# Kernel tuning notes

Measured on AMD Instinct MI355X. Metric: run time of the kernel, lower is better.

The kernel has to match this reference:

```python
import jax, jax.numpy as jnp
import numpy as np

B, T, E, H, D = 4, 2048, 1024, 16, 64  # batch, seq(block_size), n_embed, num_heads, hidden_dim


def setup_inputs() -> dict:
    key = jax.random.key(0)
    ks = jax.random.split(key, 10)
    s_in = 1.0 / np.sqrt(E)
    return {
        "x": jax.random.normal(ks[0], (B, T, E), dtype=jnp.float32),
        "Wq": jax.random.normal(ks[1], (H, E, D), dtype=jnp.float32) * s_in,
        "bq": jnp.zeros((H, D), dtype=jnp.float32),
        "Wk": jax.random.normal(ks[2], (H, E, D), dtype=jnp.float32) * s_in,
        "bk": jnp.zeros((H, D), dtype=jnp.float32),
        "Wv": jax.random.normal(ks[3], (H, E, D), dtype=jnp.float32) * s_in,
        "bv": jnp.zeros((H, D), dtype=jnp.float32),
        "Wp": jax.random.normal(ks[4], (E, E), dtype=jnp.float32) * s_in,
        "bp": jnp.zeros((E,), dtype=jnp.float32),
    }


def reference(x, Wq, bq, Wk, bk, Wv, bv, Wp, bp):
    # Batched equivalent of the per-head Python loop: each head h computes
    # causal scaled-dot-product attention with its own Q/K/V projections.
    q = jnp.einsum("bte,hed->bhtd", x, Wq) + bq[None, :, None, :]
    k = jnp.einsum("bte,hed->bhtd", x, Wk) + bk[None, :, None, :]
    v = jnp.einsum("bte,hed->bhtd", x, Wv) + bv[None, :, None, :]
    scale = 1.0 / jnp.sqrt(jnp.asarray(D, dtype=x.dtype))
    scores = jnp.einsum("bhtd,bhsd->bhts", q, k) * scale  # [B,H,T,T]
    causal = jnp.tril(jnp.ones((T, T), dtype=bool))
    scores = jnp.where(causal[None, None, :, :], scores, jnp.asarray(-jnp.inf, dtype=x.dtype))
    att = jax.nn.softmax(scores, axis=-1)
    head_out = jnp.einsum("bhts,bhsd->bhtd", att, v)  # [B,H,T,D]
    # concat heads along last dim: [B,T,H*D] == [B,T,E]
    cat = head_out.transpose(0, 2, 1, 3).reshape(B, T, H * D)
    out = cat @ Wp + bp  # final projection (dropout is identity in eval)
    return out
```

## Files before the change

kernel.cpp:

```cpp
#include <hip/hip_runtime.h>


typedef __attribute__((ext_vector_type(8))) __bf16 bf16x8;
typedef __attribute__((ext_vector_type(4))) float f32x4;
typedef __attribute__((ext_vector_type(16))) float f32x16;
typedef __attribute__((ext_vector_type(4))) unsigned int u32x4;
typedef __attribute__((ext_vector_type(2))) unsigned int u32x2;
typedef unsigned short u16;
typedef unsigned int u32;

#define DEV __device__ __forceinline__

#define QK_SCALE 0.18033688011112042f

DEV u16 f2bf(float f) {
  u32 u = __builtin_bit_cast(u32, f);
  u += 0x7fffu + ((u >> 16) & 1u);
  return (u16)(u >> 16);
}
DEV u32 pack2(float a, float b) { return (u32)f2bf(a) | ((u32)f2bf(b) << 16); }

DEV float exp2_hw(float x) { float r; asm("v_exp_f32 %0, %1" : "=v"(r) : "v"(x)); return r; }
DEV u32 cvtpk_bf16(float lo, float hi) {
  u32 r; asm("v_cvt_pk_bf16_f32 %0, %1, %2" : "=v"(r) : "v"(lo), "v"(hi)); return r;
}
DEV void pl32swap(u32& a, u32& b) { asm("v_permlane32_swap_b32 %0, %1" : "+v"(a), "+v"(b)); }
DEV float max3f(float a, float b, float c) {
  float r; asm("v_max3_f32 %0, %1, %2, %3" : "=v"(r) : "v"(a), "v"(b), "v"(c)); return r;
}

DEV f32x16 zero16() { f32x16 z;
#pragma unroll
  for (int i = 0; i < 16; i++) z[i] = 0.f;
  return z; }

__global__ __launch_bounds__(256) void prep_x_kernel(
    const float* __restrict__ x, const float* __restrict__ bq, const float* __restrict__ bk,
    const float* __restrict__ bv, u16* __restrict__ xbf, float* __restrict__ bqkv) {
  int gid = blockIdx.x * 256 + threadIdx.x;
  if (gid < 3072) {
    float v = (gid < 1024) ? bq[gid] * QK_SCALE : (gid < 2048 ? bk[gid - 1024] : bv[gid - 2048]);
    bqkv[gid] = v;
  }
  const float4* xv = (const float4*)x;
  float4 f0 = xv[(size_t)gid * 2];
  float4 f1 = xv[(size_t)gid * 2 + 1];
  u32x4 st;
  st.x = pack2(f0.x, f0.y); st.y = pack2(f0.z, f0.w);
  st.z = pack2(f1.x, f1.y); st.w = pack2(f1.z, f1.w);
  *(u32x4*)&xbf[(size_t)gid * 8] = st;
}

__global__ __launch_bounds__(256) void prep_w_kernel(
    const float* __restrict__ Wq, const float* __restrict__ Wk, const float* __restrict__ Wv,
    const float* __restrict__ Wp, u16* __restrict__ wqkvT, u16* __restrict__ wpT) {
  __shared__ float t[64][65];
  int bid = blockIdx.x, tid = threadIdx.x;
  int r0 = tid >> 6, c = tid & 63;
  if (bid < 768) {
    int p = bid >> 8, rem = bid & 255, h = rem >> 4, et = rem & 15;
    float sc = (p == 0) ? QK_SCALE : 1.0f;
    const float* src = (p == 0 ? Wq : (p == 1 ? Wk : Wv)) + ((size_t)h * 1024 + et * 64) * 64;
#pragma unroll
    for (int i = 0; i < 16; i++) { int e = r0 + i * 4; t[e][c] = src[(size_t)e * 64 + c]; }
    __syncthreads();
    u16* dst = wqkvT + ((size_t)p * 1024 + h * 64) * 1024 + et * 64;
#pragma unroll
    for (int i = 0; i < 16; i++) { int d = r0 + i * 4; dst[(size_t)d * 1024 + c] = f2bf(t[c][d] * sc); }
  } else {
    int b2 = bid - 768, rt = b2 >> 4, ct = b2 & 15;
#pragma unroll
    for (int i = 0; i < 16; i++) { int e = r0 + i * 4; t[e][c] = Wp[(size_t)(rt * 64 + e) * 1024 + ct * 64 + c]; }
    __syncthreads();
#pragma unroll
    for (int i = 0; i < 16; i++) { int f = r0 + i * 4; wpT[(size_t)(ct * 64 + f) * 1024 + rt * 64 + c] = f2bf(t[c][f]); }
  }
}

DEV void stage_tile(const u16* __restrict__ X, int row0, int k0, u16* lds, int tid) {
#pragma unroll
  for (int j = 0; j < 4; j++) {
    int ci = j * 256 + tid;
    int row = ci >> 3, slot = ci & 7;
    int srcslot = slot ^ (row & 7);
    const u16* gp = X + (size_t)(row0 + row) * 1024 + k0 + srcslot * 8;
    __builtin_amdgcn_global_load_lds((const __attribute__((address_space(1))) void*)gp,
                                     (__attribute__((address_space(3))) void*)(lds + ci * 8),
                                     16, 0, 0);
  }
}

__global__ __launch_bounds__(256, 2) void gemm128_kernel(
    const u16* __restrict__ A, const u16* __restrict__ Bt, const float* __restrict__ bias,
    int tilesN, int mode, u16* __restrict__ Qb, u16* __restrict__ Kb, u16* __restrict__ VTb,
    float* __restrict__ outF) {
  __shared__ u16 As[2][128 * 64];
  __shared__ u16 Bs[2][128 * 64];
  int nwg = gridDim.x;
  int bid = blockIdx.x;
  int swz = (bid % 8) * (nwg / 8) + bid / 8;
  int bm = swz / tilesN, bn = swz % tilesN;
  int tid = threadIdx.x;
  int lane = tid & 63, wave = tid >> 6;
  int wm = wave >> 1, wn = wave & 1;
  int lr = lane & 15, lg = lane >> 4;

  f32x4 acc[4][4];
#pragma unroll
  for (int i = 0; i < 4; i++)
#pragma unroll
    for (int j = 0; j < 4; j++) acc[i][j] = f32x4{0.f, 0.f, 0.f, 0.f};

  stage_tile(A, bm * 128, 0, As[0], tid);
  stage_tile(Bt, bn * 128, 0, Bs[0], tid);
  __syncthreads();
  int cur = 0;

  for (int t = 0; t < 16; ++t) {
    if (t + 1 < 16) {
      stage_tile(A, bm * 128, (t + 1) * 64, As[cur ^ 1], tid);
      stage_tile(Bt, bn * 128, (t + 1) * 64, Bs[cur ^ 1], tid);
    }
#pragma unroll
    for (int kf = 0; kf < 2; kf++) {
      bf16x8 af[4], bfr[4];
#pragma unroll
      for (int i = 0; i < 4; i++) {
        int ra = wm * 64 + i * 16 + lr;
        af[i] = *(const bf16x8*)&As[cur][ra * 64 + (((lg + kf * 4) ^ (ra & 7)) * 8)];
        int rb = wn * 64 + i * 16 + lr;
        bfr[i] = *(const bf16x8*)&Bs[cur][rb * 64 + (((lg + kf * 4) ^ (rb & 7)) * 8)];
      }
      __builtin_amdgcn_s_setprio(1);
#pragma unroll
      for (int i = 0; i < 4; i++)
#pragma unroll
        for (int j = 0; j < 4; j++)
          acc[i][j] = __builtin_amdgcn_mfma_f32_16x16x32_bf16(af[i], bfr[j], acc[i][j], 0, 0, 0);
      __builtin_amdgcn_s_setprio(0);
    }
    __syncthreads();
    cur ^= 1;
  }

  int crow = bm * 128 + wm * 64;
  int ccol = bn * 128 + wn * 64;
  if (mode == 0) {
#pragma unroll
    for (int j = 0; j < 4; j++) {
      int col = ccol + j * 16 + lr;
      float bb = bias[col];
      int p = col >> 10, h = (col >> 6) & 15, d = col & 63;
#pragma unroll
      for (int i = 0; i < 4; i++) {
        int row0 = crow + i * 16 + lg * 4;
        int b_ = row0 >> 11, t0 = row0 & 2047;
        if (p == 2) {
          u32x2 pv;
          pv.x = pack2(acc[i][j][0] + bb, acc[i][j][1] + bb);
          pv.y = pack2(acc[i][j][2] + bb, acc[i][j][3] + bb);
          *(u32x2*)&VTb[((size_t)(b_ * 16 + h) * 64 + d) * 2048 + t0] = pv;
        } else {
          u16* dst = (p == 0 ? Qb : Kb);
#pragma unroll
          for (int r = 0; r < 4; r++)
            dst[((size_t)(b_ * 16 + h) * 2048 + (t0 + r)) * 64 + d] = f2bf(acc[i][j][r] + bb);
        }
      }
    }
  } else {
#pragma unroll
    for (int j = 0; j < 4; j++) {
      int col = ccol + j * 16 + lr;
      float bb = bias[col];
#pragma unroll
      for (int i = 0; i < 4; i++) {
        int row0 = crow + i * 16 + lg * 4;
#pragma unroll
        for (int r = 0; r < 4; r++)
          outF[(size_t)(row0 + r) * 1024 + col] = acc[i][j][r] + bb;
      }
    }
  }
}

DEV void stage_kv256(const u16* __restrict__ Kh, const u16* __restrict__ Vh, int kv0,
                     u16* Ksb, u16* Vsb, int tid) {
#pragma unroll
  for (int j = 0; j < 2; j++) {
    int ci = j * 256 + tid;
    int row = ci >> 3, slot = ci & 7;
    int ss = slot ^ (row & 7);
    __builtin_amdgcn_global_load_lds(
        (const __attribute__((address_space(1))) void*)(Kh + (size_t)(kv0 + row) * 64 + ss * 8),
        (__attribute__((address_space(3))) void*)(Ksb + ci * 8), 16, 0, 0);
    __builtin_amdgcn_global_load_lds(
        (const __attribute__((address_space(1))) void*)(Vh + (size_t)row * 2048 + kv0 + ss * 8),
        (__attribute__((address_space(3))) void*)(Vsb + ci * 8), 16, 0, 0);
  }
}

__global__ __launch_bounds__(256, 2) void attn_kernel(
    const u16* __restrict__ Qb, const u16* __restrict__ Kb, const u16* __restrict__ VTb,
    u16* __restrict__ cat) {
  __shared__ u16 Ks[2][64 * 64];
  __shared__ u16 Vs[2][64 * 64];
  int bid = blockIdx.x;
  int t = 15 - (bid >> 6);
  int bh = bid & 63;
  int b = bh >> 4, h = bh & 15;
  int tid = threadIdx.x, wave = tid >> 6, lane = tid & 63;
  int l31 = lane & 31, hi = lane >> 5;
  int q0w = t * 128 + wave * 32;
  int qrow = q0w + l31;

  const u16* Qh = Qb + (size_t)bh * 2048 * 64;
  const u16* Kh = Kb + (size_t)bh * 2048 * 64;
  const u16* Vh = VTb + (size_t)bh * 64 * 2048;

  bf16x8 qf[4];
#pragma unroll
  for (int ks = 0; ks < 4; ks++)
    qf[ks] = *(const bf16x8*)&Qh[(size_t)qrow * 64 + ks * 16 + hi * 8];

  u32 loff[4];
#pragma unroll
  for (int ks = 0; ks < 4; ks++)
    loff[ks] = (u32)(l31 * 128 + (((ks * 2 + hi) ^ (l31 & 7)) * 16));

  f32x16 o0 = zero16(), o1 = zero16();
  float m_run = -1e30f, l_run = 0.f;
  int iters = 2 * t + 2;

  stage_kv256(Kh, Vh, 0, Ks[0], Vs[0], tid);
  __syncthreads();
  int cur = 0;

  for (int kvt = 0; kvt < iters; ++kvt) {
    int kv0 = kvt * 64;
    if (kvt + 1 < iters) stage_kv256(Kh, Vh, kv0 + 64, Ks[cur ^ 1], Vs[cur ^ 1], tid);

    if (kv0 <= q0w + 31) {
      f32x16 s0 = zero16(), s1 = zero16();
      const char* kb = (const char*)&Ks[cur][0];
      __builtin_amdgcn_s_setprio(1);
#pragma unroll
      for (int ks = 0; ks < 4; ks++) {
        bf16x8 k0 = *(const bf16x8*)(kb + loff[ks]);
        bf16x8 k1 = *(const bf16x8*)(kb + loff[ks] + 4096);
        s0 = __builtin_amdgcn_mfma_f32_32x32x16_bf16(k0, qf[ks], s0, 0, 0, 0);
        s1 = __builtin_amdgcn_mfma_f32_32x32x16_bf16(k1, qf[ks], s1, 0, 0, 0);
      }
      __builtin_amdgcn_s_setprio(0);

      if (kv0 + 63 > q0w) {
        int relh = qrow - kv0 - 4 * hi;
#pragma unroll
        for (int r = 0; r < 16; r++) {
          int off = (r & 3) + 8 * (r >> 2);
          s0[r] = (off > relh) ? -1e30f : s0[r];
          s1[r] = (off + 32 > relh) ? -1e30f : s1[r];
        }
      }

      float ta = max3f(s0[0], s0[1], s0[2]);
      float tb = max3f(s0[4], s0[5], s0[6]);
      float tc = max3f(s0[8], s0[9], s0[10]);
      float td = max3f(s0[12], s0[13], s0[14]);
      ta = max3f(ta, s0[3], s1[0]);
      tb = max3f(tb, s0[7], s1[4]);
      tc = max3f(tc, s0[11], s1[8]);
      td = max3f(td, s0[15], s1[12]);
      ta = max3f(ta, s1[1], s1[2]);
      tb = max3f(tb, s1[5], s1[6]);
      tc = max3f(tc, s1[9], s1[10]);
      td = max3f(td, s1[13], s1[14]);
      ta = max3f(ta, s1[3], tb);
      tc = max3f(tc, s1[7], td);
      float tmax = max3f(ta, tc, s1[11]);
      tmax = fmaxf(tmax, s1[15]);
      tmax = fmaxf(tmax, __shfl_xor(tmax, 32));
      float corr = 1.f;
      if (!__all(tmax <= m_run + 8.f)) {
        float m_new = fmaxf(m_run, tmax);
        corr = exp2_hw(m_run - m_new);
        o0 = o0 * corr;
        o1 = o1 * corr;
        m_run = m_new;
      }
      float t0 = 0.f, t1 = 0.f, t2 = 0.f, t3 = 0.f;
#pragma unroll
      for (int j = 0; j < 4; j++) {
        float p00 = exp2_hw(s0[j * 4 + 0] - m_run); s0[j * 4 + 0] = p00; t0 += p00;
        float p01 = exp2_hw(s0[j * 4 + 1] - m_run); s0[j * 4 + 1] = p01; t1 += p01;
        float p02 = exp2_hw(s0[j * 4 + 2] - m_run); s0[j * 4 + 2] = p02; t2 += p02;
        float p03 = exp2_hw(s0[j * 4 + 3] - m_run); s0[j * 4 + 3] = p03; t3 += p03;
        float p10 = exp2_hw(s1[j * 4 + 0] - m_run); s1[j * 4 + 0] = p10; t0 += p10;
        float p11 = exp2_hw(s1[j * 4 + 1] - m_run); s1[j * 4 + 1] = p11; t1 += p11;
        float p12 = exp2_hw(s1[j * 4 + 2] - m_run); s1[j * 4 + 2] = p12; t2 += p12;
        float p13 = exp2_hw(s1[j * 4 + 3] - m_run); s1[j * 4 + 3] = p13; t3 += p13;
      }
      float ts = (t0 + t1) + (t2 + t3);
      ts += __shfl_xor(ts, 32);
      l_run = l_run * corr + ts;

      const char* vb = (const char*)&Vs[cur][0];
      __builtin_amdgcn_s_setprio(1);
#pragma unroll
      for (int ks = 0; ks < 4; ks++) {
        const f32x16& sb = (ks < 2) ? s0 : s1;
        int g2 = (ks & 1) * 8;
        u32 a  = cvtpk_bf16(sb[g2 + 0], sb[g2 + 1]);
        u32 c  = cvtpk_bf16(sb[g2 + 2], sb[g2 + 3]);
        u32 bb = cvtpk_bf16(sb[g2 + 4], sb[g2 + 5]);
        u32 d  = cvtpk_bf16(sb[g2 + 6], sb[g2 + 7]);
        pl32swap(a, bb);
        pl32swap(c, d);
        u32x4 wv; wv.x = a; wv.y = c; wv.z = bb; wv.w = d;
        bf16x8 pf = __builtin_bit_cast(bf16x8, wv);
        bf16x8 v0 = *(const bf16x8*)(vb + loff[ks]);
        bf16x8 v1 = *(const bf16x8*)(vb + loff[ks] + 4096);
        o0 = __builtin_amdgcn_mfma_f32_32x32x16_bf16(v0, pf, o0, 0, 0, 0);
        o1 = __builtin_amdgcn_mfma_f32_32x32x16_bf16(v1, pf, o1, 0, 0, 0);
      }
      __builtin_amdgcn_s_setprio(0);
    }

    __syncthreads();
    cur ^= 1;
  }

  float li = 1.0f / l_run;
#pragma unroll
  for (int m = 0; m < 8; m++) {
    int dbase = 2 * (m & 1) + 8 * (m >> 1) + 4 * hi;
    u32 w0 = cvtpk_bf16(o0[2 * m] * li, o0[2 * m + 1] * li);
    u32 w1 = cvtpk_bf16(o1[2 * m] * li, o1[2 * m + 1] * li);
    *(u32*)&cat[(size_t)(b * 2048 + qrow) * 1024 + h * 64 + dbase] = w0;
    *(u32*)&cat[(size_t)(b * 2048 + qrow) * 1024 + h * 64 + 32 + dbase] = w1;
  }
}

extern "C" void kernel_launch(void* const* d_in, const int* in_sizes, int n_in,
                              void* d_out, int out_size, void* d_ws, size_t ws_size,
                              hipStream_t stream) {
  const float* x  = (const float*)d_in[0];
  const float* Wq = (const float*)d_in[1];
  const float* bq = (const float*)d_in[2];
  const float* Wk = (const float*)d_in[3];
  const float* bk = (const float*)d_in[4];
  const float* Wv = (const float*)d_in[5];
  const float* bv = (const float*)d_in[6];
  const float* Wp = (const float*)d_in[7];
  const float* bp = (const float*)d_in[8];

  char* w = (char*)d_ws;
  u16* xbf    = (u16*)w;                 w += (size_t)8192 * 1024 * 2;
  u16* wqkvT  = (u16*)w;                 w += (size_t)3072 * 1024 * 2;
  u16* wpT    = (u16*)w;                 w += (size_t)1024 * 1024 * 2;
  float* bqkv = (float*)w;               w += (size_t)3072 * 4;
  u16* Qb     = (u16*)w;                 w += (size_t)64 * 2048 * 64 * 2;
  u16* Kb     = (u16*)w;                 w += (size_t)64 * 2048 * 64 * 2;
  u16* VTb    = (u16*)w;                 w += (size_t)64 * 64 * 2048 * 2;
  u16* cat    = (u16*)w;                 w += (size_t)8192 * 1024 * 2;

  prep_x_kernel<<<4096, 256, 0, stream>>>(x, bq, bk, bv, xbf, bqkv);
  prep_w_kernel<<<1024, 256, 0, stream>>>(Wq, Wk, Wv, Wp, wqkvT, wpT);
  gemm128_kernel<<<1536, 256, 0, stream>>>(xbf, wqkvT, bqkv, 24, 0, Qb, Kb, VTb, nullptr);
  attn_kernel<<<1024, 256, 0, stream>>>(Qb, Kb, VTb, cat);
  gemm128_kernel<<<512, 256, 0, stream>>>(cat, wpT, bp, 8, 1, nullptr, nullptr, nullptr, (float*)d_out);
}
```

Baseline: 152.2 us.

## Load GEMM A operand directly from global into registers, drop A LDS staging

The A tile in the projection GEMM no longer goes through LDS. Each wave now loads its A fragments straight from global memory into registers, double-buffered across K steps, and the loop is unrolled by two so the register buffers alternate. The aim is to halve LDS traffic and shared-memory footprint, which may raise occupancy and remove LDS read latency for A. The cost is more VGPRs and uncoalesced, redundant global loads, since the two waves sharing a row block both fetch the same A data.

```diff
diff --git a/kernel.cpp b/kernel.cpp
--- a/kernel.cpp
+++ b/kernel.cpp
@@ -94,7 +94,6 @@
     const u16* __restrict__ A, const u16* __restrict__ Bt, const float* __restrict__ bias,
     int tilesN, int mode, u16* __restrict__ Qb, u16* __restrict__ Kb, u16* __restrict__ VTb,
     float* __restrict__ outF) {
-  __shared__ u16 As[2][128 * 64];
   __shared__ u16 Bs[2][128 * 64];
   int nwg = gridDim.x;
   int bid = blockIdx.x;
@@ -104,6 +103,8 @@
   int lane = tid & 63, wave = tid >> 6;
   int wm = wave >> 1, wn = wave & 1;
   int lr = lane & 15, lg = lane >> 4;
+  int aRowBase = bm * 128 + wm * 64;
+  const u16* Arow = A + (size_t)(aRowBase + lr) * 1024 + lg * 8;
 
   f32x4 acc[4][4];
 #pragma unroll
@@ -111,23 +112,30 @@
 #pragma unroll
     for (int j = 0; j < 4; j++) acc[i][j] = f32x4{0.f, 0.f, 0.f, 0.f};
 
-  stage_tile(A, bm * 128, 0, As[0], tid);
+  bf16x8 afA[4][2], afB[4][2];
+  auto loadA = [&](bf16x8 (&af)[4][2], int k0) {
+#pragma unroll
+    for (int i = 0; i < 4; i++)
+#pragma unroll
+      for (int kf = 0; kf < 2; kf++)
+        af[i][kf] = *(const bf16x8*)&Arow[(size_t)i * 16 * 1024 + k0 + kf * 32];
+  };
+
+  loadA(afA, 0);
   stage_tile(Bt, bn * 128, 0, Bs[0], tid);
   __syncthreads();
-  int cur = 0;
-
-  for (int t = 0; t < 16; ++t) {
+
+  auto body = [&](int t, bf16x8 (&afC)[4][2], bf16x8 (&afN)[4][2]) {
+    int cur = t & 1;
     if (t + 1 < 16) {
-      stage_tile(A, bm * 128, (t + 1) * 64, As[cur ^ 1], tid);
       stage_tile(Bt, bn * 128, (t + 1) * 64, Bs[cur ^ 1], tid);
+      loadA(afN, (t + 1) * 64);
     }
 #pragma unroll
     for (int kf = 0; kf < 2; kf++) {
-      bf16x8 af[4], bfr[4];
+      bf16x8 bfr[4];
 #pragma unroll
       for (int i = 0; i < 4; i++) {
-        int ra = wm * 64 + i * 16 + lr;
-        af[i] = *(const bf16x8*)&As[cur][ra * 64 + (((lg + kf * 4) ^ (ra & 7)) * 8)];
         int rb = wn * 64 + i * 16 + lr;
         bfr[i] = *(const bf16x8*)&Bs[cur][rb * 64 + (((lg + kf * 4) ^ (rb & 7)) * 8)];
       }
@@ -136,11 +144,16 @@
       for (int i = 0; i < 4; i++)
 #pragma unroll
         for (int j = 0; j < 4; j++)
-          acc[i][j] = __builtin_amdgcn_mfma_f32_16x16x32_bf16(af[i], bfr[j], acc[i][j], 0, 0, 0);
+          acc[i][j] = __builtin_amdgcn_mfma_f32_16x16x32_bf16(afC[i][kf], bfr[j], acc[i][j], 0, 0, 0);
       __builtin_amdgcn_s_setprio(0);
     }
     __syncthreads();
-    cur ^= 1;
+  };
+
+#pragma unroll 1
+  for (int tt = 0; tt < 8; ++tt) {
+    body(2 * tt, afA, afB);
+    body(2 * tt + 1, afB, afA);
   }
 
   int crow = bm * 128 + wm * 64;
```

Result: slower. 228.1 us (+49.9%).

## Halve GEMM K-tile to 32 for higher occupancy and merge prep kernels

Applied to the files above, without the earlier changes.

The GEMM LDS tiles shrink from K=64 to K=32. The swizzle now packs two rows per 64-element line, and the fragment offsets are precomputed once. Launch bounds rise to 4 workgroups per CU, trading twice as many k-iterations and barriers for more resident waves to hide latency. The x-conversion and weight-transpose prep kernels are merged into one launch to remove a kernel boundary.

```diff
diff --git a/kernel.cpp b/kernel.cpp
--- a/kernel.cpp
+++ b/kernel.cpp
@@ -34,28 +34,34 @@
   for (int i = 0; i < 16; i++) z[i] = 0.f;
   return z; }
 
-__global__ __launch_bounds__(256) void prep_x_kernel(
+DEV void gll16(const u16* g, u16* l) {
+  __builtin_amdgcn_global_load_lds((const __attribute__((address_space(1))) void*)g,
+                                   (__attribute__((address_space(3))) void*)l, 16, 0, 0);
+}
+
+__global__ __launch_bounds__(256) void prep_all_kernel(
     const float* __restrict__ x, const float* __restrict__ bq, const float* __restrict__ bk,
-    const float* __restrict__ bv, u16* __restrict__ xbf, float* __restrict__ bqkv) {
-  int gid = blockIdx.x * 256 + threadIdx.x;
-  if (gid < 3072) {
-    float v = (gid < 1024) ? bq[gid] * QK_SCALE : (gid < 2048 ? bk[gid - 1024] : bv[gid - 2048]);
-    bqkv[gid] = v;
-  }
-  const float4* xv = (const float4*)x;
-  float4 f0 = xv[(size_t)gid * 2];
-  float4 f1 = xv[(size_t)gid * 2 + 1];
-  u32x4 st;
-  st.x = pack2(f0.x, f0.y); st.y = pack2(f0.z, f0.w);
-  st.z = pack2(f1.x, f1.y); st.w = pack2(f1.z, f1.w);
-  *(u32x4*)&xbf[(size_t)gid * 8] = st;
-}
-
-__global__ __launch_bounds__(256) void prep_w_kernel(
-    const float* __restrict__ Wq, const float* __restrict__ Wk, const float* __restrict__ Wv,
-    const float* __restrict__ Wp, u16* __restrict__ wqkvT, u16* __restrict__ wpT) {
+    const float* __restrict__ bv, const float* __restrict__ Wq, const float* __restrict__ Wk,
+    const float* __restrict__ Wv, const float* __restrict__ Wp,
+    u16* __restrict__ xbf, float* __restrict__ bqkv, u16* __restrict__ wqkvT, u16* __restrict__ wpT) {
   __shared__ float t[64][65];
-  int bid = blockIdx.x, tid = threadIdx.x;
+  int bidAll = blockIdx.x, tid = threadIdx.x;
+  if (bidAll < 4096) {
+    int gid = bidAll * 256 + tid;
+    if (gid < 3072) {
+      float v = (gid < 1024) ? bq[gid] * QK_SCALE : (gid < 2048 ? bk[gid - 1024] : bv[gid - 2048]);
+      bqkv[gid] = v;
+    }
+    const float4* xv = (const float4*)x;
+    float4 f0 = xv[(size_t)gid * 2];
+    float4 f1 = xv[(size_t)gid * 2 + 1];
+    u32x4 st;
+    st.x = pack2(f0.x, f0.y); st.y = pack2(f0.z, f0.w);
+    st.z = pack2(f1.x, f1.y); st.w = pack2(f1.z, f1.w);
+    *(u32x4*)&xbf[(size_t)gid * 8] = st;
+    return;
+  }
+  int bid = bidAll - 4096;
   int r0 = tid >> 6, c = tid & 63;
   if (bid < 768) {
     int p = bid >> 8, rem = bid & 255, h = rem >> 4, et = rem & 15;
@@ -77,25 +83,27 @@
   }
 }
 
-DEV void stage_tile(const u16* __restrict__ X, int row0, int k0, u16* lds, int tid) {
-#pragma unroll
-  for (int j = 0; j < 4; j++) {
+DEV void stage_tile32(const u16* __restrict__ X, int row0, int k0, u16* lds, int tid) {
+#pragma unroll
+  for (int j = 0; j < 2; j++) {
     int ci = j * 256 + tid;
-    int row = ci >> 3, slot = ci & 7;
-    int srcslot = slot ^ (row & 7);
-    const u16* gp = X + (size_t)(row0 + row) * 1024 + k0 + srcslot * 8;
-    __builtin_amdgcn_global_load_lds((const __attribute__((address_space(1))) void*)gp,
-                                     (__attribute__((address_space(3))) void*)(lds + ci * 8),
-                                     16, 0, 0);
-  }
-}
-
-__global__ __launch_bounds__(256, 2) void gemm128_kernel(
+    int L = ci >> 3, half = (ci >> 2) & 1, s = ci & 3;
+    int row = L * 2 + half;
+    int srcslot = s ^ (L & 3);
+    gll16(X + (size_t)(row0 + row) * 1024 + k0 + srcslot * 8, lds + ci * 8);
+  }
+}
+
+DEV int frag_off32(int row, int lg) {
+  return (row >> 1) * 64 + (row & 1) * 32 + ((lg ^ ((row >> 1) & 3)) * 8);
+}
+
+__global__ __launch_bounds__(256, 4) void gemm128_kernel(
     const u16* __restrict__ A, const u16* __restrict__ Bt, const float* __restrict__ bias,
     int tilesN, int mode, u16* __restrict__ Qb, u16* __restrict__ Kb, u16* __restrict__ VTb,
     float* __restrict__ outF) {
-  __shared__ u16 As[2][128 * 64];
-  __shared__ u16 Bs[2][128 * 64];
+  __shared__ u16 As[2][128 * 32];
+  __shared__ u16 Bs[2][128 * 32];
   int nwg = gridDim.x;
   int bid = blockIdx.x;
   int swz = (bid % 8) * (nwg / 8) + bid / 8;
@@ -111,34 +119,36 @@
 #pragma unroll
     for (int j = 0; j < 4; j++) acc[i][j] = f32x4{0.f, 0.f, 0.f, 0.f};
 
-  stage_tile(A, bm * 128, 0, As[0], tid);
-  stage_tile(Bt, bn * 128, 0, Bs[0], tid);
+  int aoff[4], boff[4];
+#pragma unroll
+  for (int i = 0; i < 4; i++) {
+    aoff[i] = frag_off32(wm * 64 + i * 16 + lr, lg);
+    boff[i] = frag_off32(wn * 64 + i * 16 + lr, lg);
+  }
+
+  stage_tile32(A, bm * 128, 0, As[0], tid);
+  stage_tile32(Bt, bn * 128, 0, Bs[0], tid);
   __syncthreads();
   int cur = 0;
 
-  for (int t = 0; t < 16; ++t) {
-    if (t + 1 < 16) {
-      stage_tile(A, bm * 128, (t + 1) * 64, As[cur ^ 1], tid);
-      stage_tile(Bt, bn * 128, (t + 1) * 64, Bs[cur ^ 1], tid);
-    }
-#pragma unroll
-    for (int kf = 0; kf < 2; kf++) {
-      bf16x8 af[4], bfr[4];
-#pragma unroll
-      for (int i = 0; i < 4; i++) {
-        int ra = wm * 64 + i * 16 + lr;
-        af[i] = *(const bf16x8*)&As[cur][ra * 64 + (((lg + kf * 4) ^ (ra & 7)) * 8)];
-        int rb = wn * 64 + i * 16 + lr;
-        bfr[i] = *(const bf16x8*)&Bs[cur][rb * 64 + (((lg + kf * 4) ^ (rb & 7)) * 8)];
-      }
-      __builtin_amdgcn_s_setprio(1);
-#pragma unroll
-      for (int i = 0; i < 4; i++)
-#pragma unroll
-        for (int j = 0; j < 4; j++)
-          acc[i][j] = __builtin_amdgcn_mfma_f32_16x16x32_bf16(af[i], bfr[j], acc[i][j], 0, 0, 0);
-      __builtin_amdgcn_s_setprio(0);
-    }
+  for (int t = 0; t < 32; ++t) {
+    if (t + 1 < 32) {
+      stage_tile32(A, bm * 128, (t + 1) * 32, As[cur ^ 1], tid);
+      stage_tile32(Bt, bn * 128, (t + 1) * 32, Bs[cur ^ 1], tid);
+    }
+    bf16x8 af[4], bfr[4];
+#pragma unroll
+    for (int i = 0; i < 4; i++) {
+      af[i] = *(const bf16x8*)&As[cur][aoff[i]];
+      bfr[i] = *(const bf16x8*)&Bs[cur][boff[i]];
+    }
+    __builtin_amdgcn_s_setprio(1);
+#pragma unroll
+    for (int i = 0; i < 4; i++)
+#pragma unroll
+      for (int j = 0; j < 4; j++)
+        acc[i][j] = __builtin_amdgcn_mfma_f32_16x16x32_bf16(af[i], bfr[j], acc[i][j], 0, 0, 0);
+    __builtin_amdgcn_s_setprio(0);
     __syncthreads();
     cur ^= 1;
   }
@@ -364,8 +374,7 @@
   u16* VTb    = (u16*)w;                 w += (size_t)64 * 64 * 2048 * 2;
   u16* cat    = (u16*)w;                 w += (size_t)8192 * 1024 * 2;
 
-  prep_x_kernel<<<4096, 256, 0, stream>>>(x, bq, bk, bv, xbf, bqkv);
-  prep_w_kernel<<<1024, 256, 0, stream>>>(Wq, Wk, Wv, Wp, wqkvT, wpT);
+  prep_all_kernel<<<5120, 256, 0, stream>>>(x, bq, bk, bv, Wq, Wk, Wv, Wp, xbf, bqkv, wqkvT, wpT);
   gemm128_kernel<<<1536, 256, 0, stream>>>(xbf, wqkvT, bqkv, 24, 0, Qb, Kb, VTb, nullptr);
   attn_kernel<<<1024, 256, 0, stream>>>(Qb, Kb, VTb, cat);
   gemm128_kernel<<<512, 256, 0, stream>>>(cat, wpT, bp, 8, 1, nullptr, nullptr, nullptr, (float*)d_out);
```

Result: slower. 160.6 us (+5.5%).
